# Optimization experiments

Hardware: AMD Instinct MI355X
Metric: run time of the kernel (lower is better)

## Reference

```python
import jax, jax.numpy as jnp
import numpy as np

B, S, H, E, K = 4, 4096, 2048, 64, 8
SEQ_ALPHA = 0.01


def setup_inputs() -> dict:
    key = jax.random.key(0)
    k1, k2 = jax.random.split(key)
    x = jax.random.normal(k1, (B, S, H), dtype=jnp.float32)
    # kaiming_uniform_(a=sqrt(5)) on [E, H] -> bound = 1/sqrt(H)
    bound = 1.0 / np.sqrt(H)
    weight = jax.random.uniform(k2, (E, H), dtype=jnp.float32, minval=-bound, maxval=bound)
    expert_bias = jnp.zeros((E,), dtype=jnp.float32)
    return {"x": x, "weight": weight, "expert_bias": expert_bias}


def reference(x, weight, expert_bias):
    bsz, seq_len, _ = x.shape
    x_flat = x.reshape(-1, x.shape[-1])                      # [T, H], T = B*S
    logits = x_flat @ weight.T                               # [T, E]
    scores = jax.nn.sigmoid(logits)
    biased_logits = logits + expert_bias[None, :]
    _, topk_idx = jax.lax.top_k(biased_logits, K)            # [T, K] int32
    topk_w = jnp.take_along_axis(scores, topk_idx, axis=-1)  # [T, K]
    topk_w = topk_w / (topk_w.sum(axis=-1, keepdims=True) + 1e-10)  # K > 1
    # load stats (training-mode bincount)
    expert_load = jnp.bincount(topk_idx.reshape(-1), length=E).astype(jnp.int64)
    # sequence-wise balance loss (DeepSeek-V3)
    scores_r = scores.reshape(bsz, seq_len, E)
    expert_mask = jax.nn.one_hot(topk_idx.reshape(bsz, -1), E, dtype=scores.dtype)  # [B, S*K, E]
    f_i = expert_mask.sum(axis=1) / (K * seq_len)            # [B, E]
    normalized = scores_r / (scores_r.sum(axis=2, keepdims=True) + 1e-10)
    P_i = normalized.mean(axis=1)                            # [B, E]
    aux_seq_loss = SEQ_ALPHA * (f_i * P_i).sum(axis=1).mean()
    return (topk_idx, topk_w, aux_seq_loss, expert_load)
```

## Files before the change

### kernel.cpp

```cpp
#include <hip/hip_runtime.h>
#include <math.h>

#define HDIM 2048
#define TTOK 16384
#define NEXP 64
#define TOPK 8
#define SLEN 4096
#define NBATCH 4
#define PARTSZ (NEXP * TTOK)

#define OFF_W    131072
#define OFF_LOSS 262144
#define OFF_LOAD 262145

#define WS_PACC 0
#define WS_CACC 8192
#define WS_WT   16384
#define WS_PART (16384 + HDIM * NEXP)
#define EPI_NBLK 512

__global__ __launch_bounds__(256) void transpose_w(const float* __restrict__ W,
                                                   float* __restrict__ Wt,
                                                   float* __restrict__ wsz) {
  __shared__ float tile[64][65];
  const int tid = threadIdx.x;
  const int k0 = blockIdx.x * 64;
  if (blockIdx.x == 0) {
    const float4 z = {0.f, 0.f, 0.f, 0.f};
    float4* wz4 = (float4*)wsz;
#pragma unroll
    for (int i = 0; i < 16; ++i) wz4[tid + (i << 8)] = z;
  }
  {
    const int kc = (tid & 15) << 2;
    const int er = tid >> 4;
#pragma unroll
    for (int i = 0; i < 4; ++i) {
      int e = er + i * 16;
      float4 v = *(const float4*)(W + (size_t)e * HDIM + k0 + kc);
      tile[e][kc + 0] = v.x; tile[e][kc + 1] = v.y;
      tile[e][kc + 2] = v.z; tile[e][kc + 3] = v.w;
    }
  }
  __syncthreads();
  {
    const int e4 = (tid & 15) << 2;
    const int kr = tid >> 4;
#pragma unroll
    for (int i = 0; i < 4; ++i) {
      int k = kr + i * 16;
      float4 v;
      v.x = tile[e4 + 0][k]; v.y = tile[e4 + 1][k];
      v.z = tile[e4 + 2][k]; v.w = tile[e4 + 3][k];
      *(float4*)(Wt + (size_t)(k0 + k) * NEXP + e4) = v;
    }
  }
}

template <int KS>
__global__ __launch_bounds__(512, 8) void gate_gemm(
    const float* __restrict__ x,
    const float* __restrict__ Wt,
    float* __restrict__ part) {
  constexpr int KR = HDIM / KS;
  constexpr int NT = KR / 32;
  __shared__ float xs[2][128 * 32];

  const int tid = threadIdx.x;
  const int lane = tid & 63;
  const int wv = __builtin_amdgcn_readfirstlane(tid >> 6);
  const int eg = wv & 3;
  const int th = wv >> 2;
  const int bid = blockIdx.x;
  const int kh = bid & (KS - 1);
  const int tg = bid >> (KS == 8 ? 3 : 2);
  const int tok0 = tg << 7;
  const int kb = kh * KR;

  float acc[16];
#pragma unroll
  for (int j = 0; j < 16; ++j) acc[j] = 0.f;

  const int r0 = tid >> 3;
  const int sg = tid & 7;
  const int sslot = (sg ^ (r0 & 7)) << 2;
  const float* xp0 = x + (size_t)(tok0 + r0) * HDIM + kb + (sg << 2);
  const float* xp1 = xp0 + (size_t)64 * HDIM;
  float4 a0 = *(const float4*)xp0;
  float4 a1 = *(const float4*)xp1;

  const int myrow = (th << 6) + lane;
  const int rbase = myrow << 5;
  const int rs = lane & 7;

  for (int kt = 0; kt < NT; ++kt) {
    float* xb = &xs[kt & 1][0];
    *(float4*)&xb[(r0 << 5) + sslot] = a0;
    *(float4*)&xb[((r0 + 64) << 5) + sslot] = a1;
    __syncthreads();
    if (kt + 1 < NT) {
      a0 = *(const float4*)(xp0 + ((kt + 1) << 5));
      a1 = *(const float4*)(xp1 + ((kt + 1) << 5));
    }
    const float* wkb = Wt + ((size_t)(kb + (kt << 5)) << 6) + (eg << 4);
#pragma unroll
    for (int c = 0; c < 8; ++c) {
      float4 xv = *(const float4*)&xb[rbase + ((c ^ rs) << 2)];
      const float xf[4] = {xv.x, xv.y, xv.z, xv.w};
#pragma unroll
      for (int q = 0; q < 4; ++q) {
        const float* wr = wkb + (((c << 2) + q) << 6);
#pragma unroll
        for (int j = 0; j < 16; ++j) acc[j] = fmaf(xf[q], wr[j], acc[j]);
      }
    }
  }

  float* dst = part + (size_t)kh * PARTSZ + ((size_t)(eg << 4)) * TTOK + tok0 +
               (th << 6) + lane;
#pragma unroll
  for (int j = 0; j < 16; ++j) dst[(size_t)j * TTOK] = acc[j];
}

template <int KS>
__global__ __launch_bounds__(256) void gate_epilogue(
    const float* __restrict__ part, const float* __restrict__ bias,
    float* __restrict__ out, float* __restrict__ Pacc,
    float* __restrict__ Cacc) {
  __shared__ float le[64][33];
  __shared__ float rinv_sh[32];
  __shared__ unsigned csum[64];

  const int tid = threadIdx.x;
  const int t0 = blockIdx.x << 5;

  if (tid < 64) csum[tid] = 0u;

  {
    const int e = tid >> 2;
    const int tq = (tid & 3) << 2;
    float4 v[2][KS];
#pragma unroll
    for (int h = 0; h < 2; ++h) {
      const float* p = part + (size_t)e * TTOK + t0 + (h << 4) + tq;
#pragma unroll
      for (int s = 0; s < KS; ++s)
        v[h][s] = *(const float4*)(p + (size_t)s * PARTSZ);
    }
#pragma unroll
    for (int h = 0; h < 2; ++h) {
      float4 r;
      if (KS == 8) {
        r.x = ((v[h][0].x + v[h][1].x) + (v[h][2].x + v[h][3].x)) +
              ((v[h][4].x + v[h][5].x) + (v[h][6].x + v[h][7].x));
        r.y = ((v[h][0].y + v[h][1].y) + (v[h][2].y + v[h][3].y)) +
              ((v[h][4].y + v[h][5].y) + (v[h][6].y + v[h][7].y));
        r.z = ((v[h][0].z + v[h][1].z) + (v[h][2].z + v[h][3].z)) +
              ((v[h][4].z + v[h][5].z) + (v[h][6].z + v[h][7].z));
        r.w = ((v[h][0].w + v[h][1].w) + (v[h][2].w + v[h][3].w)) +
              ((v[h][4].w + v[h][5].w) + (v[h][6].w + v[h][7].w));
      } else {
        r.x = (v[h][0].x + v[h][1].x) + (v[h][2].x + v[h][3].x);
        r.y = (v[h][0].y + v[h][1].y) + (v[h][2].y + v[h][3].y);
        r.z = (v[h][0].z + v[h][1].z) + (v[h][2].z + v[h][3].z);
        r.w = (v[h][0].w + v[h][1].w) + (v[h][2].w + v[h][3].w);
      }
      const int toff = (h << 4) + tq;
      le[e][toff + 0] = r.x; le[e][toff + 1] = r.y;
      le[e][toff + 2] = r.z; le[e][toff + 3] = r.w;
    }
  }
  __syncthreads();

  const int b = (int)(blockIdx.x >> 7);

  if (tid < 32) {
    const int t = tid;
    float bl[64];
    float ssum = 0.f;
#pragma unroll
    for (int e = 0; e < NEXP; ++e) {
      float l = le[e][t];
      ssum += 1.f / (1.f + expf(-l));
      bl[e] = l + bias[e];
    }
    rinv_sh[t] = 1.f / (ssum + 1e-10f);

    unsigned long long chosen = 0ull;
    int i8[TOPK];
    float w8[TOPK];
    float wsum = 0.f;
#pragma unroll
    for (int j = 0; j < TOPK; ++j) {
      float best = -1e30f;
      int bi = 0;
      float braw = 0.f;
#pragma unroll
      for (int e = 0; e < NEXP; ++e) {
        bool ok = (((chosen >> e) & 1ull) == 0ull) && (bl[e] > best);
        if (ok) { best = bl[e]; bi = e; braw = bl[e] - bias[e]; }
      }
      chosen |= (1ull << bi);
      float sc = 1.f / (1.f + expf(-braw));
      i8[j] = bi;
      w8[j] = sc;
      wsum += sc;
    }
    const float inv = 1.f / (wsum + 1e-10f);
    const int t1 = t0 + t;
    float4 o;
    o.x = (float)i8[0]; o.y = (float)i8[1]; o.z = (float)i8[2]; o.w = (float)i8[3];
    *(float4*)(out + (size_t)t1 * TOPK) = o;
    o.x = (float)i8[4]; o.y = (float)i8[5]; o.z = (float)i8[6]; o.w = (float)i8[7];
    *(float4*)(out + (size_t)t1 * TOPK + 4) = o;
    o.x = w8[0] * inv; o.y = w8[1] * inv; o.z = w8[2] * inv; o.w = w8[3] * inv;
    *(float4*)(out + OFF_W + (size_t)t1 * TOPK) = o;
    o.x = w8[4] * inv; o.y = w8[5] * inv; o.z = w8[6] * inv; o.w = w8[7] * inv;
    *(float4*)(out + OFF_W + (size_t)t1 * TOPK + 4) = o;
#pragma unroll
    for (int j = 0; j < TOPK; ++j) atomicAdd(&csum[i8[j]], 1u);
  }

  if (tid < 64) {
    const int e = tid;
    float p = 0.f;
#pragma unroll
    for (int tt = 0; tt < 32; ++tt) {
      float sc = 1.f / (1.f + expf(-le[e][tt]));
      p += sc * rinv_sh[tt];
    }
    atomicAdd(&Pacc[(size_t)((b << 6) + e) << 5], p);
    atomicAdd(&Cacc[(size_t)((b << 6) + e) << 5], (float)csum[e]);
  }
}

__global__ __launch_bounds__(64) void gate_finalize(
    const float* __restrict__ Pacc, const float* __restrict__ Cacc,
    float* __restrict__ out) {
  const int e = threadIdx.x;
  float load = 0.f, partl = 0.f;
#pragma unroll
  for (int bb = 0; bb < NBATCH; ++bb) {
    float c = Cacc[(size_t)((bb << 6) + e) << 5];
    float p = Pacc[(size_t)((bb << 6) + e) << 5];
    load += c;
    partl += (c * (1.f / (TOPK * (float)SLEN))) * (p * (1.f / (float)SLEN));
  }
  out[OFF_LOAD + e] = load;
#pragma unroll
  for (int off = 32; off; off >>= 1) partl += __shfl_down(partl, off);
  if (e == 0) out[OFF_LOSS] = 0.01f * partl * (1.f / (float)NBATCH);
}

extern "C" void kernel_launch(void* const* d_in, const int* in_sizes, int n_in,
                              void* d_out, int out_size, void* d_ws, size_t ws_size,
                              hipStream_t stream) {
  const float* x = (const float*)d_in[0];
  const float* W = (const float*)d_in[1];
  const float* bias = (const float*)d_in[2];
  float* out = (float*)d_out;

  float* ws = (float*)d_ws;
  float* Pacc = ws + WS_PACC;
  float* Cacc = ws + WS_CACC;
  float* Wt = ws + WS_WT;
  float* part = ws + WS_PART;

  transpose_w<<<32, 256, 0, stream>>>(W, Wt, ws);

  const size_t need8 = ((size_t)WS_PART + 8 * (size_t)PARTSZ) * sizeof(float);
  if (ws_size >= need8) {
    gate_gemm<8><<<1024, 512, 0, stream>>>(x, Wt, part);
    gate_epilogue<8><<<EPI_NBLK, 256, 0, stream>>>(part, bias, out, Pacc, Cacc);
  } else {
    gate_gemm<4><<<512, 512, 0, stream>>>(x, Wt, part);
    gate_epilogue<4><<<EPI_NBLK, 256, 0, stream>>>(part, bias, out, Pacc, Cacc);
  }
  gate_finalize<<<1, 64, 0, stream>>>(Pacc, Cacc, out);
}
```

Measured before the change: 263.0 us.

## Parallelize epilogue top-k across wavefront lanes with ballot/shuffle reductions

Rewrites the gating epilogue so each wavefront processes one token at a time with one expert per lane. Softmax-normalizer sums and top-k selection use cross-lane shuffles and ballot, replacing the serial per-thread 64-expert scan in which only 32 threads did the work. Blocks now cover 64 tokens with 512 threads, and per-expert statistics are reduced through shared memory before the atomics. This adds many shuffle reductions per token (eight max-reductions for top-k) but uses the whole block instead of leaving most threads idle.

```diff
diff --git a/kernel.cpp b/kernel.cpp
--- a/kernel.cpp
+++ b/kernel.cpp
@@ -17,7 +17,7 @@
 #define WS_CACC 8192
 #define WS_WT   16384
 #define WS_PART (16384 + HDIM * NEXP)
-#define EPI_NBLK 512
+#define EPI_NBLK 256
 
 __global__ __launch_bounds__(256) void transpose_w(const float* __restrict__ W,
                                                    float* __restrict__ Wt,
@@ -122,115 +122,106 @@
   for (int j = 0; j < 16; ++j) dst[(size_t)j * TTOK] = acc[j];
 }
 
+#define WRED_SUM(v) { v += __shfl_xor(v, 1);  v += __shfl_xor(v, 2);  \
+                      v += __shfl_xor(v, 4);  v += __shfl_xor(v, 8);  \
+                      v += __shfl_xor(v, 16); v += __shfl_xor(v, 32); }
+#define WRED_MAX(v) { v = fmaxf(v, __shfl_xor(v, 1));  v = fmaxf(v, __shfl_xor(v, 2));  \
+                      v = fmaxf(v, __shfl_xor(v, 4));  v = fmaxf(v, __shfl_xor(v, 8));  \
+                      v = fmaxf(v, __shfl_xor(v, 16)); v = fmaxf(v, __shfl_xor(v, 32)); }
+#define PICK(IJ, WJ) {                                                    \
+    float m_ = cand; WRED_MAX(m_);                                        \
+    unsigned long long mk_ = __ballot(cand == m_);                        \
+    int win_ = (int)__ffsll(mk_) - 1;                                     \
+    float bw_ = __shfl(bias_r, win_);                                     \
+    WJ = 1.f / (1.f + expf(-(m_ - bw_)));                                 \
+    wsum += WJ; IJ = win_;                                                \
+    if (lane == win_) { cand = -1e30f; cnt += 1.f; } }
+
 template <int KS>
-__global__ __launch_bounds__(256) void gate_epilogue(
+__global__ __launch_bounds__(512) void gate_epilogue(
     const float* __restrict__ part, const float* __restrict__ bias,
     float* __restrict__ out, float* __restrict__ Pacc,
     float* __restrict__ Cacc) {
-  __shared__ float le[64][33];
-  __shared__ float rinv_sh[32];
-  __shared__ unsigned csum[64];
+  __shared__ float le[64 * 65];
+  __shared__ float psum_sh[8][64];
+  __shared__ float cnt_sh[8][64];
 
   const int tid = threadIdx.x;
-  const int t0 = blockIdx.x << 5;
-
-  if (tid < 64) csum[tid] = 0u;
+  const int lane = tid & 63;
+  const int wv = tid >> 6;
+  const int t0 = blockIdx.x << 6;
 
   {
-    const int e = tid >> 2;
-    const int tq = (tid & 3) << 2;
-    float4 v[2][KS];
-#pragma unroll
-    for (int h = 0; h < 2; ++h) {
-      const float* p = part + (size_t)e * TTOK + t0 + (h << 4) + tq;
-#pragma unroll
-      for (int s = 0; s < KS; ++s)
-        v[h][s] = *(const float4*)(p + (size_t)s * PARTSZ);
-    }
-#pragma unroll
-    for (int h = 0; h < 2; ++h) {
+    const int e = tid >> 3;
+    const int tsub = tid & 7;
+#pragma unroll
+    for (int w = 0; w < 2; ++w) {
+      const int tq = (tsub << 3) + (w << 2);
+      const float* p = part + (size_t)e * TTOK + t0 + tq;
+      float4 v[KS];
+#pragma unroll
+      for (int s = 0; s < KS; ++s) v[s] = *(const float4*)(p + (size_t)s * PARTSZ);
       float4 r;
       if (KS == 8) {
-        r.x = ((v[h][0].x + v[h][1].x) + (v[h][2].x + v[h][3].x)) +
-              ((v[h][4].x + v[h][5].x) + (v[h][6].x + v[h][7].x));
-        r.y = ((v[h][0].y + v[h][1].y) + (v[h][2].y + v[h][3].y)) +
-              ((v[h][4].y + v[h][5].y) + (v[h][6].y + v[h][7].y));
-        r.z = ((v[h][0].z + v[h][1].z) + (v[h][2].z + v[h][3].z)) +
-              ((v[h][4].z + v[h][5].z) + (v[h][6].z + v[h][7].z));
-        r.w = ((v[h][0].w + v[h][1].w) + (v[h][2].w + v[h][3].w)) +
-              ((v[h][4].w + v[h][5].w) + (v[h][6].w + v[h][7].w));
+        r.x = ((v[0].x + v[1].x) + (v[2].x + v[3].x)) + ((v[4].x + v[5].x) + (v[6].x + v[7].x));
+        r.y = ((v[0].y + v[1].y) + (v[2].y + v[3].y)) + ((v[4].y + v[5].y) + (v[6].y + v[7].y));
+        r.z = ((v[0].z + v[1].z) + (v[2].z + v[3].z)) + ((v[4].z + v[5].z) + (v[6].z + v[7].z));
+        r.w = ((v[0].w + v[1].w) + (v[2].w + v[3].w)) + ((v[4].w + v[5].w) + (v[6].w + v[7].w));
       } else {
-        r.x = (v[h][0].x + v[h][1].x) + (v[h][2].x + v[h][3].x);
-        r.y = (v[h][0].y + v[h][1].y) + (v[h][2].y + v[h][3].y);
-        r.z = (v[h][0].z + v[h][1].z) + (v[h][2].z + v[h][3].z);
-        r.w = (v[h][0].w + v[h][1].w) + (v[h][2].w + v[h][3].w);
+        r.x = (v[0].x + v[1].x) + (v[2].x + v[3].x);
+        r.y = (v[0].y + v[1].y) + (v[2].y + v[3].y);
+        r.z = (v[0].z + v[1].z) + (v[2].z + v[3].z);
+        r.w = (v[0].w + v[1].w) + (v[2].w + v[3].w);
       }
-      const int toff = (h << 4) + tq;
-      le[e][toff + 0] = r.x; le[e][toff + 1] = r.y;
-      le[e][toff + 2] = r.z; le[e][toff + 3] = r.w;
+      le[(tq + 0) * 65 + e] = r.x; le[(tq + 1) * 65 + e] = r.y;
+      le[(tq + 2) * 65 + e] = r.z; le[(tq + 3) * 65 + e] = r.w;
     }
   }
   __syncthreads();
 
-  const int b = (int)(blockIdx.x >> 7);
-
-  if (tid < 32) {
-    const int t = tid;
-    float bl[64];
-    float ssum = 0.f;
-#pragma unroll
-    for (int e = 0; e < NEXP; ++e) {
-      float l = le[e][t];
-      ssum += 1.f / (1.f + expf(-l));
-      bl[e] = l + bias[e];
-    }
-    rinv_sh[t] = 1.f / (ssum + 1e-10f);
-
-    unsigned long long chosen = 0ull;
-    int i8[TOPK];
-    float w8[TOPK];
+  const float bias_r = bias[lane];
+  float p_acc = 0.f, cnt = 0.f;
+
+  for (int t = (wv << 3); t < (wv << 3) + 8; ++t) {
+    float l = le[t * 65 + lane];
+    float s = 1.f / (1.f + expf(-l));
+    float ss = s;
+    WRED_SUM(ss);
+    p_acc += s * (1.f / (ss + 1e-10f));
+
+    float cand = l + bias_r;
     float wsum = 0.f;
-#pragma unroll
-    for (int j = 0; j < TOPK; ++j) {
-      float best = -1e30f;
-      int bi = 0;
-      float braw = 0.f;
-#pragma unroll
-      for (int e = 0; e < NEXP; ++e) {
-        bool ok = (((chosen >> e) & 1ull) == 0ull) && (bl[e] > best);
-        if (ok) { best = bl[e]; bi = e; braw = bl[e] - bias[e]; }
-      }
-      chosen |= (1ull << bi);
-      float sc = 1.f / (1.f + expf(-braw));
-      i8[j] = bi;
-      w8[j] = sc;
-      wsum += sc;
-    }
-    const float inv = 1.f / (wsum + 1e-10f);
-    const int t1 = t0 + t;
-    float4 o;
-    o.x = (float)i8[0]; o.y = (float)i8[1]; o.z = (float)i8[2]; o.w = (float)i8[3];
-    *(float4*)(out + (size_t)t1 * TOPK) = o;
-    o.x = (float)i8[4]; o.y = (float)i8[5]; o.z = (float)i8[6]; o.w = (float)i8[7];
-    *(float4*)(out + (size_t)t1 * TOPK + 4) = o;
-    o.x = w8[0] * inv; o.y = w8[1] * inv; o.z = w8[2] * inv; o.w = w8[3] * inv;
-    *(float4*)(out + OFF_W + (size_t)t1 * TOPK) = o;
-    o.x = w8[4] * inv; o.y = w8[5] * inv; o.z = w8[6] * inv; o.w = w8[7] * inv;
-    *(float4*)(out + OFF_W + (size_t)t1 * TOPK + 4) = o;
-#pragma unroll
-    for (int j = 0; j < TOPK; ++j) atomicAdd(&csum[i8[j]], 1u);
-  }
+    int i0, i1, i2, i3, i4, i5, i6, i7;
+    float w0, w1, w2, w3, w4, w5, w6, w7;
+    PICK(i0, w0); PICK(i1, w1); PICK(i2, w2); PICK(i3, w3);
+    PICK(i4, w4); PICK(i5, w5); PICK(i6, w6); PICK(i7, w7);
+
+    if (lane == 0) {
+      const float inv = 1.f / (wsum + 1e-10f);
+      const int t1 = t0 + t;
+      float4 o;
+      o.x = (float)i0; o.y = (float)i1; o.z = (float)i2; o.w = (float)i3;
+      *(float4*)(out + (size_t)t1 * TOPK) = o;
+      o.x = (float)i4; o.y = (float)i5; o.z = (float)i6; o.w = (float)i7;
+      *(float4*)(out + (size_t)t1 * TOPK + 4) = o;
+      o.x = w0 * inv; o.y = w1 * inv; o.z = w2 * inv; o.w = w3 * inv;
+      *(float4*)(out + OFF_W + (size_t)t1 * TOPK) = o;
+      o.x = w4 * inv; o.y = w5 * inv; o.z = w6 * inv; o.w = w7 * inv;
+      *(float4*)(out + OFF_W + (size_t)t1 * TOPK + 4) = o;
+    }
+  }
+
+  psum_sh[wv][lane] = p_acc;
+  cnt_sh[wv][lane] = cnt;
+  __syncthreads();
 
   if (tid < 64) {
-    const int e = tid;
-    float p = 0.f;
-#pragma unroll
-    for (int tt = 0; tt < 32; ++tt) {
-      float sc = 1.f / (1.f + expf(-le[e][tt]));
-      p += sc * rinv_sh[tt];
-    }
-    atomicAdd(&Pacc[(size_t)((b << 6) + e) << 5], p);
-    atomicAdd(&Cacc[(size_t)((b << 6) + e) << 5], (float)csum[e]);
+    const int b = (int)(blockIdx.x >> 6);
+    float p = 0.f, c = 0.f;
+#pragma unroll
+    for (int w = 0; w < 8; ++w) { p += psum_sh[w][tid]; c += cnt_sh[w][tid]; }
+    atomicAdd(&Pacc[(size_t)((b << 6) + tid) << 5], p);
+    atomicAdd(&Cacc[(size_t)((b << 6) + tid) << 5], c);
   }
 }
 
@@ -271,10 +262,10 @@
   const size_t need8 = ((size_t)WS_PART + 8 * (size_t)PARTSZ) * sizeof(float);
   if (ws_size >= need8) {
     gate_gemm<8><<<1024, 512, 0, stream>>>(x, Wt, part);
-    gate_epilogue<8><<<EPI_NBLK, 256, 0, stream>>>(part, bias, out, Pacc, Cacc);
+    gate_epilogue<8><<<EPI_NBLK, 512, 0, stream>>>(part, bias, out, Pacc, Cacc);
   } else {
     gate_gemm<4><<<512, 512, 0, stream>>>(x, Wt, part);
-    gate_epilogue<4><<<EPI_NBLK, 256, 0, stream>>>(part, bias, out, Pacc, Cacc);
+    gate_epilogue<4><<<EPI_NBLK, 512, 0, stream>>>(part, bias, out, Pacc, Cacc);
   }
   gate_finalize<<<1, 64, 0, stream>>>(Pacc, Cacc, out);
 }
```

After: 248.6 us. -5.5%, faster.
